# Kernel tuning notes

Hardware: AMD Instinct MI355X
Metric: run time of the kernel (lower is better)

## Reference

```python
import jax, jax.numpy as jnp
import numpy as np

N_NODES = 100000
D_FEAT = 128
N_GATHER = 1600000
N_MACRO = 50000


def setup_inputs() -> dict:
    key = jax.random.key(0)
    k1, k2, k3 = jax.random.split(key, 3)
    node_feature = jax.random.normal(k1, (N_NODES, D_FEAT), dtype=jnp.float32)
    batch_node_ids = jax.random.randint(k2, (N_GATHER,), 0, N_NODES, dtype=jnp.int64 if jax.config.jax_enable_x64 else jnp.int32)
    batch_macro_node_ids = jnp.sort(jax.random.randint(k3, (N_GATHER,), 0, N_MACRO, dtype=jnp.int64 if jax.config.jax_enable_x64 else jnp.int32))
    return {
        "node_feature": node_feature,
        "batch_node_ids": batch_node_ids,
        "batch_macro_node_ids": batch_macro_node_ids,
        "num_macro_nodes": N_MACRO,
    }


def reference(node_feature, batch_node_ids, batch_macro_node_ids, num_macro_nodes):
    # gather: [n_gather, d]
    gathered = node_feature[batch_node_ids]
    # scatter-mean by segment id -> [num_macro_nodes, d]
    sums = jax.ops.segment_sum(gathered, batch_macro_node_ids, num_segments=num_macro_nodes)
    counts = jax.ops.segment_sum(
        jnp.ones((batch_macro_node_ids.shape[0],), dtype=node_feature.dtype),
        batch_macro_node_ids, num_segments=num_macro_nodes)
    # empty segments stay 0 (matches torch_scatter 'mean' behavior)
    return sums / jnp.maximum(counts, 1.0)[:, None]
```

## Files before the change

kernel.cpp:

```cpp
#include <hip/hip_runtime.h>

#define D_FEAT 128
#define MAX_CHUNK 1024

__global__ __launch_bounds__(256)
void prep_kernel(const float* __restrict__ feat,
                 unsigned char* __restrict__ tab, float* __restrict__ scales,
                 int n_nodes, int qb,
                 const int* __restrict__ mids, int n_gather,
                 int num_macro, int* __restrict__ offsets) {
    if ((int)blockIdx.x < qb) {
        const int wave = threadIdx.x >> 6;
        const int lane = threadIdx.x & 63;
        const int row  = blockIdx.x * 4 + wave;
        if (row >= n_nodes) return;
        const float2 v = ((const float2*)feat)[(size_t)row * 64 + lane];
        float a = fmaxf(fabsf(v.x), fabsf(v.y));
        #pragma unroll
        for (int d = 1; d <= 32; d <<= 1) a = fmaxf(a, __shfl_xor(a, d, 64));
        const float inv = (a > 0.f) ? (127.f / a) : 0.f;
        const int q0 = (int)rintf(v.x * inv);
        const int q1 = (int)rintf(v.y * inv);
        const unsigned short p =
            (unsigned short)((q0 & 0xFF) | ((q1 & 0xFF) << 8));
        ((unsigned short*)tab)[(size_t)row * 64 + lane] = p;
        if (lane == 0) scales[row] = a * (1.f / 127.f);
    } else {
        const int i = ((int)blockIdx.x - qb) * 256 + (int)threadIdx.x;
        if (i >= n_gather) return;
        const int cur  = mids[i];
        const int prev = (i == 0) ? -1 : mids[i - 1];
        for (int m = prev + 1; m <= cur; ++m) offsets[m] = i;
        if (i == n_gather - 1) {
            for (int m = cur + 1; m <= num_macro; ++m) offsets[m] = n_gather;
        }
    }
}

__global__ __launch_bounds__(256)
void pool_wave_i8_kernel(const unsigned char* __restrict__ tab,
                         const float* __restrict__ scales,
                         const int* __restrict__ nids,
                         const int* __restrict__ offsets,
                         float* __restrict__ out, int num_macro) {
    const int wave = threadIdx.x >> 6;
    const int m    = blockIdx.x * 4 + wave;
    if (m >= num_macro) return;

    const int lane = threadIdx.x & 63;
    const int cc   = (lane & 31) << 2;
    const int slot = lane >> 5;

    const int start = offsets[m];
    const int cnt   = offsets[m + 1] - start;

    float4 acc = make_float4(0.f, 0.f, 0.f, 0.f);

    for (int b0 = 0; b0 < cnt; b0 += 64) {
        const int rem = min(cnt - b0, 64);
        const int my  = nids[start + b0 + ((lane < rem) ? lane : rem - 1)];
        const float sc = scales[my];

        for (int k = 0; k < rem; k += 16) {
            #pragma unroll
            for (int j = 0; j < 8; ++j) {
                const int row = k + (j << 1) + slot;
                const int src = (row < rem) ? row : 0;
                const int idx = __shfl(my, src, 64);
                const float s = __shfl(sc, src, 64);
                const unsigned int w =
                    *(const unsigned int*)(tab + (size_t)idx * D_FEAT + cc);
                if (row < rem) {
                    acc.x += s * (float)(signed char)(w       & 0xFF);
                    acc.y += s * (float)(signed char)((w >> 8)  & 0xFF);
                    acc.z += s * (float)(signed char)((w >> 16) & 0xFF);
                    acc.w += s * (float)(signed char)(w >> 24);
                }
            }
        }
    }

    acc.x += __shfl_xor(acc.x, 32, 64);
    acc.y += __shfl_xor(acc.y, 32, 64);
    acc.z += __shfl_xor(acc.z, 32, 64);
    acc.w += __shfl_xor(acc.w, 32, 64);

    if (slot == 0) {
        const float inv = (cnt > 0) ? (1.0f / (float)cnt) : 0.0f;
        float4 r = make_float4(acc.x * inv, acc.y * inv, acc.z * inv, acc.w * inv);
        *(float4*)(out + (size_t)m * D_FEAT + cc) = r;
    }
}

__global__ __launch_bounds__(256)
void pool_mean_fp32_kernel(const float* __restrict__ feat,
                           const int* __restrict__ nids,
                           const int* __restrict__ offsets,
                           float* __restrict__ out) {
    const int m    = blockIdx.x;
    const int tid  = threadIdx.x;
    const int g    = tid >> 5;
    const int c4   = (tid & 31) << 2;

    const int start = offsets[m];
    const int cnt   = offsets[m + 1] - start;

    __shared__ int   s_idx[MAX_CHUNK];
    __shared__ float red[8][D_FEAT];

    float4 acc = make_float4(0.f, 0.f, 0.f, 0.f);
    for (int base = 0; base < cnt; base += MAX_CHUNK) {
        const int chunk = min(cnt - base, MAX_CHUNK);
        for (int t = tid; t < chunk; t += 256) s_idx[t] = nids[start + base + t];
        __syncthreads();
        int r = g;
        for (; r + 24 < chunk; r += 32) {
            const float4 v0 = *(const float4*)(feat + (size_t)s_idx[r]      * D_FEAT + c4);
            const float4 v1 = *(const float4*)(feat + (size_t)s_idx[r + 8]  * D_FEAT + c4);
            const float4 v2 = *(const float4*)(feat + (size_t)s_idx[r + 16] * D_FEAT + c4);
            const float4 v3 = *(const float4*)(feat + (size_t)s_idx[r + 24] * D_FEAT + c4);
            acc.x += v0.x + v1.x + v2.x + v3.x;
            acc.y += v0.y + v1.y + v2.y + v3.y;
            acc.z += v0.z + v1.z + v2.z + v3.z;
            acc.w += v0.w + v1.w + v2.w + v3.w;
        }
        for (; r < chunk; r += 8) {
            const float4 v = *(const float4*)(feat + (size_t)s_idx[r] * D_FEAT + c4);
            acc.x += v.x; acc.y += v.y; acc.z += v.z; acc.w += v.w;
        }
        __syncthreads();
    }

    red[g][c4 + 0] = acc.x;
    red[g][c4 + 1] = acc.y;
    red[g][c4 + 2] = acc.z;
    red[g][c4 + 3] = acc.w;
    __syncthreads();

    if (tid < D_FEAT) {
        float s = 0.f;
        #pragma unroll
        for (int k = 0; k < 8; ++k) s += red[k][tid];
        const float inv = (cnt > 0) ? (1.0f / (float)cnt) : 0.0f;
        out[(size_t)m * D_FEAT + tid] = s * inv;
    }
}

__global__ __launch_bounds__(256)
void seg_offsets_kernel(const int* __restrict__ mids, int n_gather,
                        int num_macro, int* __restrict__ offsets) {
    const int i = blockIdx.x * blockDim.x + threadIdx.x;
    if (i >= n_gather) return;
    const int cur  = mids[i];
    const int prev = (i == 0) ? -1 : mids[i - 1];
    for (int m = prev + 1; m <= cur; ++m) offsets[m] = i;
    if (i == n_gather - 1) {
        for (int m = cur + 1; m <= num_macro; ++m) offsets[m] = n_gather;
    }
}

extern "C" void kernel_launch(void* const* d_in, const int* in_sizes, int n_in,
                              void* d_out, int out_size, void* d_ws, size_t ws_size,
                              hipStream_t stream) {
    const float* feat = (const float*)d_in[0];
    const int*   nids = (const int*)d_in[1];
    const int*   mids = (const int*)d_in[2];
    float*       out  = (float*)d_out;

    const int n_gather  = in_sizes[1];
    const int num_macro = out_size / D_FEAT;
    const int n_nodes   = in_sizes[0] / D_FEAT;

    int* offsets = (int*)d_ws;
    const size_t off_bytes   = ((size_t)(num_macro + 1) * sizeof(int) + 255) & ~(size_t)255;
    const size_t scale_bytes = ((size_t)n_nodes * sizeof(float) + 255) & ~(size_t)255;
    const size_t tab_bytes   = (size_t)n_nodes * D_FEAT;
    const bool   use_i8      = (off_bytes + scale_bytes + tab_bytes) <= ws_size;

    if (use_i8) {
        float*         scales = (float*)((char*)d_ws + off_bytes);
        unsigned char* tab    = (unsigned char*)((char*)d_ws + off_bytes + scale_bytes);

        const int qb = (n_nodes + 3) / 4;
        const int ob = (n_gather + 255) / 256;
        prep_kernel<<<qb + ob, 256, 0, stream>>>(
            feat, tab, scales, n_nodes, qb, mids, n_gather, num_macro, offsets);

        pool_wave_i8_kernel<<<(num_macro + 3) / 4, 256, 0, stream>>>(
            tab, scales, nids, offsets, out, num_macro);
    } else {
        seg_offsets_kernel<<<(n_gather + 255) / 256, 256, 0, stream>>>(
            mids, n_gather, num_macro, offsets);
        pool_mean_fp32_kernel<<<num_macro, 256, 0, stream>>>(feat, nids, offsets, out);
    }
}
```

Measured before the change: 168.2 us.

## Split int8 table into column slices pinned per XCC with atomic work queue

Stores the quantized feature table as four column slices of 32 bytes per node, and has each workgroup read its XCC id and process only the slice for that XCC. The intent is that each XCC's L2 cache holds only a quarter of the table, so gathered rows hit cache more often. Work is handed out as groups of 8 segments through a per-slice atomic counter, with a persistent grid of 2048 blocks. The approach assumes workgroups spread evenly over XCCs, with XCC ids mapping onto 4 slices. It adds atomic traffic, re-reads indices and scales four times, and could starve or leave slices unbalanced if the XCC distribution is uneven.

```diff
diff --git a/kernel.cpp b/kernel.cpp
--- a/kernel.cpp
+++ b/kernel.cpp
@@ -1,6 +1,8 @@
 #include <hip/hip_runtime.h>
 
 #define D_FEAT 128
+#define NSLICE 4
+#define SLICE_COLS 32
 #define MAX_CHUNK 1024
 
 __global__ __launch_bounds__(256)
@@ -8,7 +10,8 @@
                  unsigned char* __restrict__ tab, float* __restrict__ scales,
                  int n_nodes, int qb,
                  const int* __restrict__ mids, int n_gather,
-                 int num_macro, int* __restrict__ offsets) {
+                 int num_macro, int* __restrict__ offsets,
+                 int* __restrict__ ctr) {
     if ((int)blockIdx.x < qb) {
         const int wave = threadIdx.x >> 6;
         const int lane = threadIdx.x & 63;
@@ -23,11 +26,16 @@
         const int q1 = (int)rintf(v.y * inv);
         const unsigned short p =
             (unsigned short)((q0 & 0xFF) | ((q1 & 0xFF) << 8));
-        ((unsigned short*)tab)[(size_t)row * 64 + lane] = p;
+        const size_t sliceBytes = (size_t)n_nodes * SLICE_COLS;
+        ((unsigned short*)(tab + (size_t)(lane >> 4) * sliceBytes
+                               + (size_t)row * SLICE_COLS))[lane & 15] = p;
         if (lane == 0) scales[row] = a * (1.f / 127.f);
     } else {
         const int i = ((int)blockIdx.x - qb) * 256 + (int)threadIdx.x;
         if (i >= n_gather) return;
+        if (i == 0) {
+            ctr[0] = 0; ctr[64] = 0; ctr[128] = 0; ctr[192] = 0;
+        }
         const int cur  = mids[i];
         const int prev = (i == 0) ? -1 : mids[i - 1];
         for (int m = prev + 1; m <= cur; ++m) offsets[m] = i;
@@ -38,57 +46,76 @@
 }
 
 __global__ __launch_bounds__(256)
-void pool_wave_i8_kernel(const unsigned char* __restrict__ tab,
-                         const float* __restrict__ scales,
-                         const int* __restrict__ nids,
-                         const int* __restrict__ offsets,
-                         float* __restrict__ out, int num_macro) {
-    const int wave = threadIdx.x >> 6;
-    const int m    = blockIdx.x * 4 + wave;
-    if (m >= num_macro) return;
-
-    const int lane = threadIdx.x & 63;
-    const int cc   = (lane & 31) << 2;
-    const int slot = lane >> 5;
-
-    const int start = offsets[m];
-    const int cnt   = offsets[m + 1] - start;
-
-    float4 acc = make_float4(0.f, 0.f, 0.f, 0.f);
-
-    for (int b0 = 0; b0 < cnt; b0 += 64) {
-        const int rem = min(cnt - b0, 64);
-        const int my  = nids[start + b0 + ((lane < rem) ? lane : rem - 1)];
-        const float sc = scales[my];
-
-        for (int k = 0; k < rem; k += 16) {
+void pool_slice_xcc_kernel(const unsigned char* __restrict__ tab,
+                           const float* __restrict__ scales,
+                           const int* __restrict__ nids,
+                           const int* __restrict__ offsets,
+                           int* __restrict__ ctr,
+                           float* __restrict__ out,
+                           int num_macro, int n_nodes) {
+    unsigned xcc;
+    asm("s_getreg_b32 %0, hwreg(HW_REG_XCC_ID, 0, 4)" : "=s"(xcc));
+    const int slice = (int)(xcc & 3u);
+    const unsigned char* __restrict__ sl =
+        tab + (size_t)slice * ((size_t)n_nodes * SLICE_COLS);
+
+    const int lane = (int)threadIdx.x & 63;
+    const int e8   = lane >> 3;
+    const int b4   = (lane & 7) << 2;
+
+    for (;;) {
+        int t0;
+        if (lane == 0) t0 = atomicAdd(&ctr[slice * 64], 1);
+        t0 = __shfl(t0, 0, 64);
+        const int m0 = t0 * 8;
+        if (m0 >= num_macro) break;
+        const int m1 = min(m0 + 8, num_macro);
+
+        for (int m = m0; m < m1; ++m) {
+            const int start = offsets[m];
+            const int cnt   = offsets[m + 1] - start;
+
+            float a0 = 0.f, a1 = 0.f, a2 = 0.f, a3 = 0.f;
+
+            for (int k = 0; k < cnt; k += 16) {
+                const int eA = k + e8;
+                const int eB = eA + 8;
+                const int gA = start + ((eA < cnt) ? eA : cnt - 1);
+                const int gB = start + ((eB < cnt) ? eB : cnt - 1);
+                const int nA = nids[gA];
+                const int nB = nids[gB];
+                float sA = scales[nA];
+                float sB = scales[nB];
+                const unsigned wA =
+                    *(const unsigned*)(sl + ((size_t)nA << 5) + b4);
+                const unsigned wB =
+                    *(const unsigned*)(sl + ((size_t)nB << 5) + b4);
+                if (eA >= cnt) sA = 0.f;
+                if (eB >= cnt) sB = 0.f;
+                a0 += sA * (float)(signed char)( wA        & 0xFF);
+                a1 += sA * (float)(signed char)((wA >> 8)  & 0xFF);
+                a2 += sA * (float)(signed char)((wA >> 16) & 0xFF);
+                a3 += sA * (float)(signed char)( wA >> 24);
+                a0 += sB * (float)(signed char)( wB        & 0xFF);
+                a1 += sB * (float)(signed char)((wB >> 8)  & 0xFF);
+                a2 += sB * (float)(signed char)((wB >> 16) & 0xFF);
+                a3 += sB * (float)(signed char)( wB >> 24);
+            }
+
             #pragma unroll
-            for (int j = 0; j < 8; ++j) {
-                const int row = k + (j << 1) + slot;
-                const int src = (row < rem) ? row : 0;
-                const int idx = __shfl(my, src, 64);
-                const float s = __shfl(sc, src, 64);
-                const unsigned int w =
-                    *(const unsigned int*)(tab + (size_t)idx * D_FEAT + cc);
-                if (row < rem) {
-                    acc.x += s * (float)(signed char)(w       & 0xFF);
-                    acc.y += s * (float)(signed char)((w >> 8)  & 0xFF);
-                    acc.z += s * (float)(signed char)((w >> 16) & 0xFF);
-                    acc.w += s * (float)(signed char)(w >> 24);
-                }
+            for (int h = 8; h <= 32; h <<= 1) {
+                a0 += __shfl_xor(a0, h, 64);
+                a1 += __shfl_xor(a1, h, 64);
+                a2 += __shfl_xor(a2, h, 64);
+                a3 += __shfl_xor(a3, h, 64);
             }
-        }
-    }
-
-    acc.x += __shfl_xor(acc.x, 32, 64);
-    acc.y += __shfl_xor(acc.y, 32, 64);
-    acc.z += __shfl_xor(acc.z, 32, 64);
-    acc.w += __shfl_xor(acc.w, 32, 64);
-
-    if (slot == 0) {
-        const float inv = (cnt > 0) ? (1.0f / (float)cnt) : 0.0f;
-        float4 r = make_float4(acc.x * inv, acc.y * inv, acc.z * inv, acc.w * inv);
-        *(float4*)(out + (size_t)m * D_FEAT + cc) = r;
+
+            if (lane < 8) {
+                const float inv = (cnt > 0) ? (1.0f / (float)cnt) : 0.0f;
+                *(float4*)(out + (size_t)m * D_FEAT + slice * SLICE_COLS + b4) =
+                    make_float4(a0 * inv, a1 * inv, a2 * inv, a3 * inv);
+            }
+        }
     }
 }
 
@@ -173,21 +200,26 @@
 
     int* offsets = (int*)d_ws;
     const size_t off_bytes   = ((size_t)(num_macro + 1) * sizeof(int) + 255) & ~(size_t)255;
+    const size_t ctr_bytes   = 4 * 64 * sizeof(int);
     const size_t scale_bytes = ((size_t)n_nodes * sizeof(float) + 255) & ~(size_t)255;
     const size_t tab_bytes   = (size_t)n_nodes * D_FEAT;
-    const bool   use_i8      = (off_bytes + scale_bytes + tab_bytes) <= ws_size;
+    const bool   use_i8      =
+        (off_bytes + ctr_bytes + scale_bytes + tab_bytes) <= ws_size;
 
     if (use_i8) {
-        float*         scales = (float*)((char*)d_ws + off_bytes);
-        unsigned char* tab    = (unsigned char*)((char*)d_ws + off_bytes + scale_bytes);
+        int*           ctr    = (int*)((char*)d_ws + off_bytes);
+        float*         scales = (float*)((char*)d_ws + off_bytes + ctr_bytes);
+        unsigned char* tab    =
+            (unsigned char*)((char*)d_ws + off_bytes + ctr_bytes + scale_bytes);
 
         const int qb = (n_nodes + 3) / 4;
         const int ob = (n_gather + 255) / 256;
         prep_kernel<<<qb + ob, 256, 0, stream>>>(
-            feat, tab, scales, n_nodes, qb, mids, n_gather, num_macro, offsets);
-
-        pool_wave_i8_kernel<<<(num_macro + 3) / 4, 256, 0, stream>>>(
-            tab, scales, nids, offsets, out, num_macro);
+            feat, tab, scales, n_nodes, qb, mids, n_gather, num_macro,
+            offsets, ctr);
+
+        pool_slice_xcc_kernel<<<2048, 256, 0, stream>>>(
+            tab, scales, nids, offsets, ctr, out, num_macro, n_nodes);
     } else {
         seg_offsets_kernel<<<(n_gather + 255) / 256, 256, 0, stream>>>(
             mids, n_gather, num_macro, offsets);
```

Result: slower. 231.4 us (+37.5%).
